# Kernel optimization log

Hardware: AMD Instinct MI355X
Metric: run time of the kernel (lower is better)

Reference implementation:

```python
import jax, jax.numpy as jnp
import numpy as np

LATENT = 256
HEADS = 4
DIM_HEAD = 256            # dim_head = latent_channels
INNER = HEADS * DIM_HEAD  # 1024
ROT_DIM = DIM_HEAD // 2   # rotary dim per coordinate (relative_emb_dim=2)
MIN_FREQ = 1.0 / 64.0     # 1/res
ROT_SCALE = 16.0          # CrossFormer scale
FF_SCALE = 0.5            # Gaussian Fourier feature scale
PI = 3.141592653589793
OUT_CH = 3


def _gelu(x):
    return jax.nn.gelu(x, approximate=False)  # torch nn.GELU default (erf)


def _rot_freqs(coords, dim):
    # coords: [b, n] -> freqs [b, n, dim]
    inv_freq = 1.0 / (10000.0 ** (jnp.arange(0, dim, 2, dtype=jnp.float32) / dim))
    t = coords * (ROT_SCALE / MIN_FREQ)
    f = t[..., None] * inv_freq               # [b, n, dim//2]
    return jnp.concatenate([f, f], axis=-1)    # [b, n, dim]


def _rotate_half(x):
    x1, x2 = jnp.split(x, 2, axis=-1)
    return jnp.concatenate([-x2, x1], axis=-1)


def _apply_rot(t, freqs):
    return t * jnp.cos(freqs) + _rotate_half(t) * jnp.sin(freqs)


def _apply_2d_rot(t, fx, fy):
    d = t.shape[-1]
    tx, ty = t[..., : d // 2], t[..., d // 2 :]
    return jnp.concatenate([_apply_rot(tx, fx), _apply_rot(ty, fy)], axis=-1)


def _inst_norm(t, eps=1e-5):
    # galerkin normalization: non-affine norm over head dim (InstanceNorm1d, affine=False)
    mu = jnp.mean(t, axis=-1, keepdims=True)
    var = jnp.var(t, axis=-1, keepdims=True)
    return (t - mu) * jax.lax.rsqrt(var + eps)


def setup_inputs() -> dict:
    key = jax.random.key(0)
    ks = jax.random.split(key, 20)
    b, nq, nc = 8, 4096, 4096
    s = 0.02
    return {
        "z": jax.random.normal(ks[0], (b, nc, LATENT), jnp.float32),
        "query_pos": jax.random.uniform(ks[1], (b, nq, 2), jnp.float32),
        "context_pos": jax.random.uniform(ks[2], (b, nc, 2), jnp.float32),
        # GaussianFourierFeatureTransform buffer B: [2, mapping_size=latent/2]
        "B_ff": jax.random.normal(ks[3], (2, LATENT // 2), jnp.float32) * FF_SCALE,
        # coordinate_projection linears (bias=False)
        "Wc1": jax.random.normal(ks[4], (LATENT, LATENT), jnp.float32) * s,
        "Wc2": jax.random.normal(ks[5], (LATENT, LATENT), jnp.float32) * s,
        # cross attention projections
        "Wq": jax.random.normal(ks[6], (LATENT, INNER), jnp.float32) * s,
        "Wkv": jax.random.normal(ks[7], (LATENT, 2 * INNER), jnp.float32) * s,
        "Wo": jax.random.normal(ks[8], (INNER, LATENT), jnp.float32) * s,
        "bo": jnp.zeros((LATENT,), jnp.float32),
        # feed-forward (mlp_dim = latent)
        "Wf1": jax.random.normal(ks[9], (LATENT, LATENT), jnp.float32) * s,
        "bf1": jnp.zeros((LATENT,), jnp.float32),
        "Wf2": jax.random.normal(ks[10], (LATENT, LATENT), jnp.float32) * s,
        "bf2": jnp.zeros((LATENT,), jnp.float32),
        # output head
        "Wh1": jax.random.normal(ks[11], (LATENT + 2, LATENT), jnp.float32) * s,
        "Wh2": jax.random.normal(ks[12], (LATENT, LATENT // 2), jnp.float32) * s,
        "Wh3": jax.random.normal(ks[13], (LATENT // 2, OUT_CH), jnp.float32) * s,
        "bh3": jnp.zeros((OUT_CH,), jnp.float32),
    }


def reference(z, query_pos, context_pos, B_ff, Wc1, Wc2, Wq, Wkv, Wo, bo,
              Wf1, bf1, Wf2, bf2, Wh1, Wh2, Wh3, bh3):
    b, nq, _ = query_pos.shape
    nc = z.shape[1]
    # 1) Gaussian Fourier features + 2-layer projection
    ff = 2.0 * PI * (query_pos @ B_ff)                           # [b, nq, latent/2]
    x = jnp.concatenate([jnp.sin(ff), jnp.cos(ff)], axis=-1)      # [b, nq, latent]
    x = _gelu(x @ Wc1) @ Wc2
    # 2) galerkin cross attention with 2D rotary relative pos emb
    q = (x @ Wq).reshape(b, nq, HEADS, DIM_HEAD).transpose(0, 2, 1, 3)
    k, v = jnp.split(z @ Wkv, 2, axis=-1)
    k = k.reshape(b, nc, HEADS, DIM_HEAD).transpose(0, 2, 1, 3)
    v = v.reshape(b, nc, HEADS, DIM_HEAD).transpose(0, 2, 1, 3)
    fxq = _rot_freqs(query_pos[..., 0], ROT_DIM)[:, None]         # [b,1,nq,rot]
    fyq = _rot_freqs(query_pos[..., 1], ROT_DIM)[:, None]
    fxk = _rot_freqs(context_pos[..., 0], ROT_DIM)[:, None]
    fyk = _rot_freqs(context_pos[..., 1], ROT_DIM)[:, None]
    q = _apply_2d_rot(q, fxq, fyq)
    k = _apply_2d_rot(k, fxk, fyk)
    k = _inst_norm(k)
    v = _inst_norm(v)
    kv = jnp.einsum('bhnd,bhne->bhde', k, v)                      # [b,h,d,d]
    attn = jnp.einsum('bhmd,bhde->bhme', q, kv) * (1.0 / nc)      # [b,h,nq,d]
    attn = attn.transpose(0, 2, 1, 3).reshape(b, nq, INNER)
    x = (attn @ Wo + bo) + x                                      # residual
    x = (_gelu(x @ Wf1 + bf1) @ Wf2 + bf2) + x                    # FFN residual
    # 3) output head on [features, coords]
    h = jnp.concatenate([x, query_pos], axis=-1)
    h = _gelu(h @ Wh1)
    h = _gelu(h @ Wh2)
    return h @ Wh3 + bh3                                          # [b, nq, out_ch]
```

## Files before the change

### kernel.cpp

```cpp
#include <hip/hip_runtime.h>
#include <math.h>


typedef unsigned short u16;
typedef __attribute__((ext_vector_type(4))) float f32x4;
typedef __attribute__((ext_vector_type(8))) short s16x8;
typedef __attribute__((ext_vector_type(8))) unsigned short u16x8;
typedef __attribute__((ext_vector_type(4))) unsigned short u16x4;

#define LOG2_1E4_D64 0.20762050593046013f

__device__ __forceinline__ u16 f2b(float f){
  union { float f; unsigned u; } v; v.f = f;
  unsigned u = v.u;
  u += 0x7FFFu + ((u >> 16) & 1u);
  return (u16)(u >> 16);
}
__device__ __forceinline__ float b2f(u16 b){
  union { unsigned u; float f; } v; v.u = ((unsigned)b) << 16; return v.f;
}
__device__ __forceinline__ float gelu_f(float x){
  return 0.5f * x * (1.0f + erff(x * 0.7071067811865475f));
}

#if __has_builtin(__builtin_amdgcn_global_load_lds)
#define HAVE_GLL 1
typedef const __attribute__((address_space(1))) void* as1cv;
typedef __attribute__((address_space(3))) void* as3v;
__device__ __forceinline__ void gload16(const void* g, void* l){
  __builtin_amdgcn_global_load_lds((as1cv)g, (as3v)l, 16, 0, 0);
}
#else
#define HAVE_GLL 0
#endif


__global__ __launch_bounds__(256) void k_cast(const float* __restrict__ in, u16* __restrict__ out){
  long i = (long)blockIdx.x * 256 + threadIdx.x;
  float4 f = ((const float4*)in)[i];
  u16x4 o = { f2b(f.x), f2b(f.y), f2b(f.z), f2b(f.w) };
  ((u16x4*)out)[i] = o;
}

struct TCArgs {
  const float* W[9]; u16* Wt[9];
  int K[9]; int N[9]; int boff[10];
};
__global__ __launch_bounds__(256) void k_tcast_all(TCArgs a){
  int b = blockIdx.x;
  int w = 0;
  while (b >= a.boff[w+1]) w++;
  int idx = (b - a.boff[w]) * 256 + threadIdx.x;
  int K = a.K[w], N = a.N[w];
  int n = idx / K, k = idx - n * K;
  a.Wt[w][idx] = f2b(a.W[w][(long)k * N + n]);
}

__global__ __launch_bounds__(256) void k_fourier(const float* __restrict__ qp, const float* __restrict__ Bff, u16* __restrict__ X0){
  int tid = threadIdx.x;
  long r = (long)blockIdx.x * 2 + (tid >> 7);
  int j = tid & 127;
  float qx = qp[r*2], qy = qp[r*2+1];
  float ff = 6.283185307179586f * (qx * Bff[j] + qy * Bff[128 + j]);
  X0[r*256 + j]       = f2b(sinf(ff));
  X0[r*256 + 128 + j] = f2b(cosf(ff));
}

__global__ __launch_bounds__(256) void k_rot_q(u16* __restrict__ Q, const float* __restrict__ qp){
  int id = blockIdx.x * 256 + threadIdx.x;
  int l = id & 63;
  int h = (id >> 6) & 3;
  long r = (unsigned)id >> 8;
  float invf = exp2f(-(float)l * LOG2_1E4_D64);
  float ax = qp[r*2]   * 1024.0f * invf;
  float ay = qp[r*2+1] * 1024.0f * invf;
  float sx = sinf(ax), cx = cosf(ax), sy = sinf(ay), cy = cosf(ay);
  long base = r*1024 + (long)h*256 + l;
  float t0 = b2f(Q[base]), t1 = b2f(Q[base+64]), t2 = b2f(Q[base+128]), t3 = b2f(Q[base+192]);
  Q[base]       = f2b(t0*cx - t1*sx);
  Q[base + 64]  = f2b(t1*cx + t0*sx);
  Q[base + 128] = f2b(t2*cy - t3*sy);
  Q[base + 192] = f2b(t3*cy + t2*sy);
}

__global__ __launch_bounds__(256) void k_kvt(const u16* __restrict__ in, const float* __restrict__ cp,
                                             u16* __restrict__ outT, int do_rot){
  __shared__ u16 sb[64*256];
  int tid  = threadIdx.x;
  int lane = tid & 63, wave = tid >> 6;
  int h = blockIdx.y;
  long n0 = (long)blockIdx.x * 64;
  int bb  = (int)(n0 >> 12);
  int nn0 = (int)(n0 & 4095);
  float invf = exp2f(-(float)lane * LOG2_1E4_D64);

  for (int rr = 0; rr < 16; rr++){
    int lrow = wave * 16 + rr;
    long n = n0 + lrow;
    long base = n * 1024 + (long)h * 256 + lane;
    float r0 = b2f(in[base]), r1 = b2f(in[base+64]), r2 = b2f(in[base+128]), r3 = b2f(in[base+192]);
    if (do_rot){
      float ax = cp[n*2]   * 1024.0f * invf;
      float ay = cp[n*2+1] * 1024.0f * invf;
      float sx = sinf(ax), cxv = cosf(ax), sy = sinf(ay), cyv = cosf(ay);
      float t0 = r0, t1 = r1, t2 = r2, t3 = r3;
      r0 = t0*cxv - t1*sx;  r1 = t1*cxv + t0*sx;
      r2 = t2*cyv - t3*sy;  r3 = t3*cyv + t2*sy;
    }
    float s1 = r0+r1+r2+r3;
    float s2 = r0*r0+r1*r1+r2*r2+r3*r3;
#pragma unroll
    for (int m = 1; m < 64; m <<= 1){ s1 += __shfl_xor(s1, m, 64); s2 += __shfl_xor(s2, m, 64); }
    float mu  = s1 * 0.00390625f;
    float var = s2 * 0.00390625f - mu*mu;
    float inv = 1.0f / sqrtf(var + 1e-5f);
    int sw = (lrow >> 2) << 1;
    sb[lrow*256 + ((lane      ) ^ sw)] = f2b((r0-mu)*inv);
    sb[lrow*256 + ((lane + 64 ) ^ sw)] = f2b((r1-mu)*inv);
    sb[lrow*256 + ((lane + 128) ^ sw)] = f2b((r2-mu)*inv);
    sb[lrow*256 + ((lane + 192) ^ sw)] = f2b((r3-mu)*inv);
  }
  __syncthreads();
  long matbase = ((long)(bb*4 + h) * 256) * 4096 + nn0;
  int n4 = (lane & 15) * 4;
  int sw = (lane & 15) << 1;
#pragma unroll
  for (int rnd = 0; rnd < 16; rnd++){
    int d = rnd*16 + wave*4 + (lane >> 4);
    u16x4 vv;
#pragma unroll
    for (int j = 0; j < 4; j++) vv[j] = sb[(n4+j)*256 + (d ^ sw)];
    *(u16x4*)(outT + matbase + (long)d*4096 + n4) = vv;
  }
}

__global__ __launch_bounds__(256) void k_red(const float* __restrict__ p, u16* __restrict__ out, long stride){
  long i = (long)blockIdx.x * 256 + threadIdx.x;
  f32x4 s = ((const f32x4*)p)[i];
  s += ((const f32x4*)(p + stride))[i];
  s += ((const f32x4*)(p + 2*stride))[i];
  s += ((const f32x4*)(p + 3*stride))[i];
  u16x4 o = { f2b(s[0]), f2b(s[1]), f2b(s[2]), f2b(s[3]) };
  ((u16x4*)out)[i] = o;
}

__global__ __launch_bounds__(256) void k_final(const u16* __restrict__ H2, const float* __restrict__ Wh3,
                                               const float* __restrict__ bh3, float* __restrict__ out){
  long r = (long)blockIdx.x * 256 + threadIdx.x;
  float a0 = bh3[0], a1 = bh3[1], a2 = bh3[2];
  const u16x8* hrow = (const u16x8*)(H2 + r*128);
#pragma unroll
  for (int c8 = 0; c8 < 16; c8++){
    u16x8 hv = hrow[c8];
#pragma unroll
    for (int e = 0; e < 8; e++){
      float f = b2f(hv[e]);
      int k = c8*8 + e;
      a0 += f * Wh3[k*3];
      a1 += f * Wh3[k*3+1];
      a2 += f * Wh3[k*3+2];
    }
  }
  out[r*3] = a0; out[r*3+1] = a1; out[r*3+2] = a2;
}


enum { EP_B = 0, EP_GELU = 1, EP_BIAS_GELU = 2, EP_BIAS_RESB = 3, EP_SCALE = 4,
       EP_T = 5, EP_QP_GELU = 6, EP_TF32 = 7 };

struct GArgs {
  const u16* A; const u16* B;
  u16* Cb; float* Cf;
  const float* bias; const u16* res; const float* qp; const float* wtail;
  float scale;
  int M, N, K, lda, ldb, ldc, NLO;
  long sAh, sAl, sBh, sBl, sCh, sCl;
};

template<int EP>
__global__ __launch_bounds__(256, 2)
void gemm_k(GArgs g){
  int z = blockIdx.z;
  int zh = z / g.NLO, zl = z - zh * g.NLO;
  const u16* A = g.A + (long)zh * g.sAh + (long)zl * g.sAl;
  const u16* B = g.B + (long)zh * g.sBh + (long)zl * g.sBl;
  long coff = (long)zh * g.sCh + (long)zl * g.sCl;

  __shared__ u16 As[128*32];
  __shared__ u16 Bs[128*32];

  int tid  = threadIdx.x;
  int lane = tid & 63;
  int wave = tid >> 6;
  int wm = (wave & 1) << 6;
  int wn = (wave >> 1) << 6;
  long m0 = (long)blockIdx.x * 128;
  long n0 = (long)blockIdx.y * 128;

  int r15 = lane & 15;
  int cc  = lane >> 4;

#if HAVE_GLL
  int rA0 = (wave*2 + 0) * 16;
  int rA1 = (wave*2 + 1) * 16;
  int srow = lane >> 2;
  int scol = (lane & 3) * 8;
  u16* lA0 = &As[rA0*32];
  u16* lA1 = &As[rA1*32];
  u16* lB0 = &Bs[rA0*32];
  u16* lB1 = &Bs[rA1*32];
  const u16* gA0 = A + (m0 + rA0 + srow) * g.lda + scol;
  const u16* gA1 = A + (m0 + rA1 + srow) * g.lda + scol;
  const u16* gB0 = B + (n0 + rA0 + srow) * g.ldb + scol;
  const u16* gB1 = B + (n0 + rA1 + srow) * g.ldb + scol;
#else
  int sm  = tid >> 2;
  int sc  = tid & 3;
  int so0 = sm * 32 + sc * 8;
  int so1 = (sm + 64) * 32 + sc * 8;
  const u16* pA0 = A + (m0 + sm ) * g.lda + sc * 8;
  const u16* pA1 = A + (m0 + sm + 64) * g.lda + sc * 8;
  const u16* pB0 = B + (n0 + sm ) * g.ldb + sc * 8;
  const u16* pB1 = B + (n0 + sm + 64) * g.ldb + sc * 8;
#endif

  f32x4 acc[4][4];
#pragma unroll
  for (int i = 0; i < 4; i++)
#pragma unroll
    for (int j = 0; j < 4; j++)
      acc[i][j] = f32x4{0.f, 0.f, 0.f, 0.f};

  for (int k0 = 0; k0 < g.K; k0 += 32){
#if HAVE_GLL
    __syncthreads();
    gload16(gA0 + k0, lA0);
    gload16(gA1 + k0, lA1);
    gload16(gB0 + k0, lB0);
    gload16(gB1 + k0, lB1);
    __syncthreads();
#else
    u16x8 va0 = *(const u16x8*)(pA0 + k0);
    u16x8 va1 = *(const u16x8*)(pA1 + k0);
    u16x8 vb0 = *(const u16x8*)(pB0 + k0);
    u16x8 vb1 = *(const u16x8*)(pB1 + k0);
    __syncthreads();
    *(u16x8*)&As[so0] = va0;
    *(u16x8*)&As[so1] = va1;
    *(u16x8*)&Bs[so0] = vb0;
    *(u16x8*)&Bs[so1] = vb1;
    __syncthreads();
#endif
    s16x8 af[4], bf[4];
#pragma unroll
    for (int i = 0; i < 4; i++) af[i] = *(const s16x8*)&As[(wm + i*16 + r15)*32 + cc*8];
#pragma unroll
    for (int i = 0; i < 4; i++) bf[i] = *(const s16x8*)&Bs[(wn + i*16 + r15)*32 + cc*8];
#pragma unroll
    for (int i = 0; i < 4; i++)
#pragma unroll
      for (int j = 0; j < 4; j++)
        acc[i][j] = __builtin_amdgcn_mfma_f32_16x16x32_bf16(af[i], bf[j], acc[i][j], 0, 0, 0);
  }

  int colb = (int)n0 + wn + r15;
  int rowb = (int)m0 + wm + cc * 4;
#pragma unroll
  for (int i = 0; i < 4; i++){
#pragma unroll
    for (int j = 0; j < 4; j++){
      int col = colb + j*16;
#pragma unroll
      for (int r = 0; r < 4; r++){
        int row = rowb + i*16 + r;
        float v = acc[i][j][r];
        if constexpr (EP == EP_B){
          g.Cb[coff + (long)row * g.ldc + col] = f2b(v);
        } else if constexpr (EP == EP_GELU){
          g.Cb[coff + (long)row * g.ldc + col] = f2b(gelu_f(v));
        } else if constexpr (EP == EP_BIAS_GELU){
          v = gelu_f(v + g.bias[col]);
          g.Cb[coff + (long)row * g.ldc + col] = f2b(v);
        } else if constexpr (EP == EP_BIAS_RESB){
          v += g.bias[col] + b2f(g.res[(long)row * g.ldc + col]);
          g.Cb[coff + (long)row * g.ldc + col] = f2b(v);
        } else if constexpr (EP == EP_SCALE){
          g.Cb[coff + (long)row * g.ldc + col] = f2b(v * g.scale);
        } else if constexpr (EP == EP_T){
          g.Cb[coff + (long)col * g.ldc + row] = f2b(v);
        } else if constexpr (EP == EP_TF32){
          g.Cf[coff + (long)col * g.ldc + row] = v;
        } else {
          v += g.qp[(long)row*2] * g.wtail[col] + g.qp[(long)row*2+1] * g.wtail[256+col];
          g.Cb[coff + (long)row * g.ldc + col] = f2b(gelu_f(v));
        }
      }
    }
  }
}


extern "C" void kernel_launch(void* const* d_in, const int* in_sizes, int n_in,
                              void* d_out, int out_size, void* d_ws, size_t ws_size,
                              hipStream_t stream){
  const float* z   = (const float*)d_in[0];
  const float* qp  = (const float*)d_in[1];
  const float* cp  = (const float*)d_in[2];
  const float* Bff = (const float*)d_in[3];
  const float* Wc1 = (const float*)d_in[4];
  const float* Wc2 = (const float*)d_in[5];
  const float* Wq  = (const float*)d_in[6];
  const float* Wkv = (const float*)d_in[7];
  const float* Wo  = (const float*)d_in[8];
  const float* bo  = (const float*)d_in[9];
  const float* Wf1 = (const float*)d_in[10];
  const float* bf1 = (const float*)d_in[11];
  const float* Wf2 = (const float*)d_in[12];
  const float* bf2 = (const float*)d_in[13];
  const float* Wh1 = (const float*)d_in[14];
  const float* Wh2 = (const float*)d_in[15];
  const float* Wh3 = (const float*)d_in[16];
  const float* bh3 = (const float*)d_in[17];
  float* out = (float*)d_out;
  (void)in_sizes; (void)n_in; (void)out_size;

  size_t mb = ws_size >> 20;
  int C;
  if      (mb >= 264) C = 1;
  else if (mb >= 168) C = 2;
  else if (mb >= 120) C = 4;
  else                C = 8;
  const int NB = 8 / C;
  const long R = (long)NB * 4096;

  char* ws = (char*)d_ws;
  const size_t MB = 1024*1024;
  u16* WqT  = (u16*)(ws + 0);
  u16* WkvT = (u16*)(ws + 512*1024);
  u16* WoT  = (u16*)(ws + 1536*1024);
  u16* Wc1T = (u16*)(ws + 2048*1024);
  u16* Wc2T = (u16*)(ws + (2048+128)*1024);
  u16* Wf1T = (u16*)(ws + (2048+256)*1024);
  u16* Wf2T = (u16*)(ws + (2048+384)*1024);
  u16* Wh1T = (u16*)(ws + (2048+512)*1024);
  u16* Wh2T = (u16*)(ws + (2048+640)*1024);
  u16* R1 = (u16*)(ws + 4*MB);
  u16* R2 = (u16*)(ws + 20*MB);
  u16* R3 = (u16*)(ws + 36*MB);
  u16* R4 = (u16*)(ws + 52*MB);
  u16* kvT = (u16*)(ws + 68*MB);
  u16* BIG1 = (u16*)(ws + 72*MB);
  u16* BIG2 = (u16*)((char*)BIG1 + (size_t)NB*8*MB);
  u16* BIG3 = (u16*)((char*)BIG2 + (size_t)NB*8*MB);

  u16* X0b = R1; u16* X2b = R1;
  u16* Tb  = R2; u16* H1b = R2;
  u16* Xb  = R3;
  u16* Zb  = R4; u16* H2b = R4;

  auto G = [&](int ep, const u16* A, const u16* B, u16* Cb, float* Cf,
               const float* bias, const u16* res, const float* qq, const float* wtail,
               float scale, int M, int N, int K, int lda, int ldb, int ldc,
               int nz, int NLO, long sAh, long sAl, long sBh, long sBl, long sCh, long sCl){
    GArgs g;
    g.A=A; g.B=B; g.Cb=Cb; g.Cf=Cf; g.bias=bias; g.res=res; g.qp=qq; g.wtail=wtail;
    g.scale=scale; g.M=M; g.N=N; g.K=K; g.lda=lda; g.ldb=ldb; g.ldc=ldc; g.NLO=NLO;
    g.sAh=sAh; g.sAl=sAl; g.sBh=sBh; g.sBl=sBl; g.sCh=sCh; g.sCl=sCl;
    dim3 gr(M/128, N/128, nz); dim3 bl(256);
    switch(ep){
      case EP_B:          gemm_k<EP_B><<<gr,bl,0,stream>>>(g); break;
      case EP_GELU:       gemm_k<EP_GELU><<<gr,bl,0,stream>>>(g); break;
      case EP_BIAS_GELU:  gemm_k<EP_BIAS_GELU><<<gr,bl,0,stream>>>(g); break;
      case EP_BIAS_RESB:  gemm_k<EP_BIAS_RESB><<<gr,bl,0,stream>>>(g); break;
      case EP_SCALE:      gemm_k<EP_SCALE><<<gr,bl,0,stream>>>(g); break;
      case EP_T:          gemm_k<EP_T><<<gr,bl,0,stream>>>(g); break;
      case EP_QP_GELU:    gemm_k<EP_QP_GELU><<<gr,bl,0,stream>>>(g); break;
      case EP_TF32:       gemm_k<EP_TF32><<<gr,bl,0,stream>>>(g); break;
    }
  };

  k_cast<<<dim3(8192), dim3(256), 0, stream>>>(z, Zb);
  {
    TCArgs a;
    const float* Ws[9] = { Wq, Wkv, Wo, Wc1, Wc2, Wf1, Wf2, Wh1, Wh2 };
    u16* Wts[9] = { WqT, WkvT, WoT, Wc1T, Wc2T, Wf1T, Wf2T, Wh1T, Wh2T };
    int Ks[9] = { 256, 256, 1024, 256, 256, 256, 256, 256, 256 };
    int Ns[9] = { 1024, 2048, 256, 256, 256, 256, 256, 256, 128 };
    int off = 0;
    for (int i = 0; i < 9; i++){
      a.W[i] = Ws[i]; a.Wt[i] = Wts[i]; a.K[i] = Ks[i]; a.N[i] = Ns[i];
      a.boff[i] = off; off += Ks[i]*Ns[i]/256;
    }
    a.boff[9] = off;
    k_tcast_all<<<dim3(off), dim3(256), 0, stream>>>(a);
  }

  k_fourier<<<dim3(16384), dim3(256), 0, stream>>>(qp, Bff, X0b);
  G(EP_GELU, X0b, Wc1T, Tb, 0, 0,0,0,0, 1.f, 32768,256,256, 256,256,256, 1,1, 0,0,0,0,0,0);
  G(EP_B,    Tb,  Wc2T, Xb, 0, 0,0,0,0, 1.f, 32768,256,256, 256,256,256, 1,1, 0,0,0,0,0,0);

  for (int c = 0; c < C; c++){
    long row0 = (long)c * R;
    const u16* Zc = Zb + row0 * 256;
    G(EP_B, Zc, WkvT, BIG1, 0, 0,0,0,0, 1.f, (int)R,1024,256, 256,256,1024, 1,1, 0,0,0,0,0,0);
    k_kvt<<<dim3((int)(R/64), 4), dim3(256), 0, stream>>>(BIG1, cp + row0*2, BIG2, 1);
    G(EP_B, Zc, WkvT + 1024*256, BIG1, 0, 0,0,0,0, 1.f, (int)R,1024,256, 256,256,1024, 1,1, 0,0,0,0,0,0);
    k_kvt<<<dim3((int)(R/64), 4), dim3(256), 0, stream>>>(BIG1, cp + row0*2, BIG3, 0);
    G(EP_TF32, BIG2, BIG3, 0, (float*)BIG1, 0,0,0,0, 1.f,
      256,256,1024, 4096,4096,256, 4*NB*4, NB*4,
      1024,1048576, 1024,1048576, (long)NB*4*65536,65536);
    k_red<<<dim3(NB*256), dim3(256), 0, stream>>>((float*)BIG1, kvT + (long)c*NB*4*65536, (long)NB*4*65536);
    G(EP_B, Xb + row0*256, WqT, BIG1, 0, 0,0,0,0, 1.f, (int)R,1024,256, 256,256,1024, 1,1, 0,0,0,0,0,0);
    k_rot_q<<<dim3((int)R), dim3(256), 0, stream>>>(BIG1, qp + row0*2);
    G(EP_SCALE, BIG1, kvT + (long)c*NB*4*65536, BIG2, 0, 0,0,0,0, 1.0f/4096.0f,
      4096,256,256, 1024,256,1024, NB*4,4, 4194304,256, 262144,65536, 4194304,256);
    G(EP_BIAS_RESB, BIG2, WoT, X2b + row0*256, 0, bo, Xb + row0*256, 0,0, 1.f,
      (int)R,256,1024, 1024,1024,256, 1,1, 0,0,0,0,0,0);
  }

  G(EP_BIAS_GELU, X2b, Wf1T, Tb, 0, bf1, 0,0,0, 1.f, 32768,256,256, 256,256,256, 1,1, 0,0,0,0,0,0);
  G(EP_BIAS_RESB, Tb, Wf2T, Xb, 0, bf2, X2b, 0,0, 1.f, 32768,256,256, 256,256,256, 1,1, 0,0,0,0,0,0);
  G(EP_QP_GELU, Xb, Wh1T, H1b, 0, 0,0, qp, Wh1 + 65536, 1.f, 32768,256,256, 256,256,256, 1,1, 0,0,0,0,0,0);
  G(EP_GELU, H1b, Wh2T, H2b, 0, 0,0,0,0, 1.f, 32768,128,256, 256,256,128, 1,1, 0,0,0,0,0,0);
  k_final<<<dim3(128), dim3(256), 0, stream>>>(H2b, Wh3, bh3, out);
}
```

Measured before the change: 648.2 us.

## Fuse K/V/Q projections with rotary, instance norm and transpose epilogues

Adds a gemm_fuse kernel that computes a full 256-wide head tile per block, so the rotary embedding and the per-row instance norm can be applied in registers. For K and V it writes the transposed layout directly, and for Q it writes the rotated result. This removes the separate k_kvt and k_rot_q passes and their intermediate global round trips. The kv GEMM now uses a non-transposed fp32 epilogue with its operand order swapped. The trade-offs are larger shared memory and register use per block, which may lower occupancy, and the switch to fast __sinf/__cosf on large angles, which may cost accuracy.

```diff
diff --git a/kernel.cpp b/kernel.cpp
--- a/kernel.cpp
+++ b/kernel.cpp
@@ -66,74 +66,6 @@
   X0[r*256 + 128 + j] = f2b(cosf(ff));
 }
 
-__global__ __launch_bounds__(256) void k_rot_q(u16* __restrict__ Q, const float* __restrict__ qp){
-  int id = blockIdx.x * 256 + threadIdx.x;
-  int l = id & 63;
-  int h = (id >> 6) & 3;
-  long r = (unsigned)id >> 8;
-  float invf = exp2f(-(float)l * LOG2_1E4_D64);
-  float ax = qp[r*2]   * 1024.0f * invf;
-  float ay = qp[r*2+1] * 1024.0f * invf;
-  float sx = sinf(ax), cx = cosf(ax), sy = sinf(ay), cy = cosf(ay);
-  long base = r*1024 + (long)h*256 + l;
-  float t0 = b2f(Q[base]), t1 = b2f(Q[base+64]), t2 = b2f(Q[base+128]), t3 = b2f(Q[base+192]);
-  Q[base]       = f2b(t0*cx - t1*sx);
-  Q[base + 64]  = f2b(t1*cx + t0*sx);
-  Q[base + 128] = f2b(t2*cy - t3*sy);
-  Q[base + 192] = f2b(t3*cy + t2*sy);
-}
-
-__global__ __launch_bounds__(256) void k_kvt(const u16* __restrict__ in, const float* __restrict__ cp,
-                                             u16* __restrict__ outT, int do_rot){
-  __shared__ u16 sb[64*256];
-  int tid  = threadIdx.x;
-  int lane = tid & 63, wave = tid >> 6;
-  int h = blockIdx.y;
-  long n0 = (long)blockIdx.x * 64;
-  int bb  = (int)(n0 >> 12);
-  int nn0 = (int)(n0 & 4095);
-  float invf = exp2f(-(float)lane * LOG2_1E4_D64);
-
-  for (int rr = 0; rr < 16; rr++){
-    int lrow = wave * 16 + rr;
-    long n = n0 + lrow;
-    long base = n * 1024 + (long)h * 256 + lane;
-    float r0 = b2f(in[base]), r1 = b2f(in[base+64]), r2 = b2f(in[base+128]), r3 = b2f(in[base+192]);
-    if (do_rot){
-      float ax = cp[n*2]   * 1024.0f * invf;
-      float ay = cp[n*2+1] * 1024.0f * invf;
-      float sx = sinf(ax), cxv = cosf(ax), sy = sinf(ay), cyv = cosf(ay);
-      float t0 = r0, t1 = r1, t2 = r2, t3 = r3;
-      r0 = t0*cxv - t1*sx;  r1 = t1*cxv + t0*sx;
-      r2 = t2*cyv - t3*sy;  r3 = t3*cyv + t2*sy;
-    }
-    float s1 = r0+r1+r2+r3;
-    float s2 = r0*r0+r1*r1+r2*r2+r3*r3;
-#pragma unroll
-    for (int m = 1; m < 64; m <<= 1){ s1 += __shfl_xor(s1, m, 64); s2 += __shfl_xor(s2, m, 64); }
-    float mu  = s1 * 0.00390625f;
-    float var = s2 * 0.00390625f - mu*mu;
-    float inv = 1.0f / sqrtf(var + 1e-5f);
-    int sw = (lrow >> 2) << 1;
-    sb[lrow*256 + ((lane      ) ^ sw)] = f2b((r0-mu)*inv);
-    sb[lrow*256 + ((lane + 64 ) ^ sw)] = f2b((r1-mu)*inv);
-    sb[lrow*256 + ((lane + 128) ^ sw)] = f2b((r2-mu)*inv);
-    sb[lrow*256 + ((lane + 192) ^ sw)] = f2b((r3-mu)*inv);
-  }
-  __syncthreads();
-  long matbase = ((long)(bb*4 + h) * 256) * 4096 + nn0;
-  int n4 = (lane & 15) * 4;
-  int sw = (lane & 15) << 1;
-#pragma unroll
-  for (int rnd = 0; rnd < 16; rnd++){
-    int d = rnd*16 + wave*4 + (lane >> 4);
-    u16x4 vv;
-#pragma unroll
-    for (int j = 0; j < 4; j++) vv[j] = sb[(n4+j)*256 + (d ^ sw)];
-    *(u16x4*)(outT + matbase + (long)d*4096 + n4) = vv;
-  }
-}
-
 __global__ __launch_bounds__(256) void k_red(const float* __restrict__ p, u16* __restrict__ out, long stride){
   long i = (long)blockIdx.x * 256 + threadIdx.x;
   f32x4 s = ((const f32x4*)p)[i];
@@ -165,8 +97,208 @@
 }
 
 
+template<int MODE>
+__global__ __launch_bounds__(256, 2)
+void gemm_fuse(const u16* __restrict__ A, const u16* __restrict__ Bw,
+               u16* __restrict__ out, const float* __restrict__ pos){
+  __shared__ u16 As[128*32];
+  __shared__ u16 Bs[256*32];
+
+  int tid  = threadIdx.x;
+  int lane = tid & 63;
+  int wave = tid >> 6;
+  int wm = (wave & 1) << 6;
+  int wn = (wave >> 1) << 7;
+  int whalf = wave >> 1;
+  int h = blockIdx.y;
+  long m0 = (long)blockIdx.x * 128;
+
+  int r15 = lane & 15;
+  int cc  = lane >> 4;
+  const u16* Bh = Bw + (long)h * 65536;
+
+#if HAVE_GLL
+  int srow = lane >> 2;
+  int scol = (lane & 3) * 8;
+  u16* lA[2]; const u16* gA[2];
+#pragma unroll
+  for (int t = 0; t < 2; t++){
+    int rb = (wave*2 + t) * 16;
+    lA[t] = &As[rb*32];
+    gA[t] = A + (m0 + rb + srow) * 256 + scol;
+  }
+  u16* lB[4]; const u16* gB[4];
+#pragma unroll
+  for (int t = 0; t < 4; t++){
+    int rb = (wave*4 + t) * 16;
+    lB[t] = &Bs[rb*32];
+    gB[t] = Bh + (rb + srow) * 256 + scol;
+  }
+#else
+  int sm  = tid >> 2;
+  int sc  = tid & 3;
+#endif
+
+  f32x4 acc[4][8];
+#pragma unroll
+  for (int i = 0; i < 4; i++)
+#pragma unroll
+    for (int j = 0; j < 8; j++)
+      acc[i][j] = f32x4{0.f, 0.f, 0.f, 0.f};
+
+  for (int k0 = 0; k0 < 256; k0 += 32){
+#if HAVE_GLL
+    __syncthreads();
+#pragma unroll
+    for (int t = 0; t < 2; t++) gload16(gA[t] + k0, lA[t]);
+#pragma unroll
+    for (int t = 0; t < 4; t++) gload16(gB[t] + k0, lB[t]);
+    __syncthreads();
+#else
+    u16x8 va = *(const u16x8*)(A + (m0 + sm)*256 + sc*8 + k0);
+    u16x8 vb0 = *(const u16x8*)(Bh + (sm      )*256 + sc*8 + k0);
+    u16x8 vb1 = *(const u16x8*)(Bh + (sm + 64 )*256 + sc*8 + k0);
+    u16x8 vb2 = *(const u16x8*)(Bh + (sm + 128)*256 + sc*8 + k0);
+    u16x8 vb3 = *(const u16x8*)(Bh + (sm + 192)*256 + sc*8 + k0);
+    u16x8 va1 = *(const u16x8*)(A + (m0 + sm + 64)*256 + sc*8 + k0);
+    __syncthreads();
+    *(u16x8*)&As[sm*32 + sc*8] = va;
+    *(u16x8*)&As[(sm+64)*32 + sc*8] = va1;
+    *(u16x8*)&Bs[sm*32 + sc*8] = vb0;
+    *(u16x8*)&Bs[(sm+64)*32 + sc*8] = vb1;
+    *(u16x8*)&Bs[(sm+128)*32 + sc*8] = vb2;
+    *(u16x8*)&Bs[(sm+192)*32 + sc*8] = vb3;
+    __syncthreads();
+#endif
+    s16x8 af[4], bf[8];
+#pragma unroll
+    for (int i = 0; i < 4; i++) af[i] = *(const s16x8*)&As[(wm + i*16 + r15)*32 + cc*8];
+#pragma unroll
+    for (int j = 0; j < 8; j++) bf[j] = *(const s16x8*)&Bs[(wn + j*16 + r15)*32 + cc*8];
+#pragma unroll
+    for (int i = 0; i < 4; i++)
+#pragma unroll
+      for (int j = 0; j < 8; j++)
+        acc[i][j] = __builtin_amdgcn_mfma_f32_16x16x32_bf16(af[i], bf[j], acc[i][j], 0, 0, 0);
+  }
+
+  if constexpr (MODE != 1){
+    float invf4[4];
+#pragma unroll
+    for (int jl = 0; jl < 4; jl++)
+      invf4[jl] = 1024.0f * exp2f(-(float)(jl*16 + r15) * LOG2_1E4_D64);
+#pragma unroll
+    for (int i = 0; i < 4; i++){
+#pragma unroll
+      for (int r = 0; r < 4; r++){
+        long n = m0 + wm + i*16 + cc*4 + r;
+        float p = pos[n*2 + whalf];
+#pragma unroll
+        for (int jl = 0; jl < 4; jl++){
+          float a = p * invf4[jl];
+          float s = __sinf(a), c = __cosf(a);
+          float t0 = acc[i][jl][r], t1 = acc[i][jl+4][r];
+          acc[i][jl][r]   = t0*c - t1*s;
+          acc[i][jl+4][r] = t1*c + t0*s;
+        }
+      }
+    }
+  }
+
+  if constexpr (MODE == 2){
+#pragma unroll
+    for (int i = 0; i < 4; i++)
+#pragma unroll
+      for (int j = 0; j < 8; j++)
+#pragma unroll
+        for (int r = 0; r < 4; r++){
+          long row = m0 + wm + i*16 + cc*4 + r;
+          int col = h*256 + wn + j*16 + r15;
+          out[row*1024 + col] = f2b(acc[i][j][r]);
+        }
+  } else {
+    __shared__ float PS1[2][128];
+    __shared__ float PS2[2][128];
+    __shared__ u16 TB[64*256];
+
+    float s1a[4][4], s2a[4][4];
+#pragma unroll
+    for (int i = 0; i < 4; i++){
+#pragma unroll
+      for (int r = 0; r < 4; r++){
+        float s1 = 0.f, s2 = 0.f;
+#pragma unroll
+        for (int j = 0; j < 8; j++){
+          float v = acc[i][j][r];
+          s1 += v; s2 += v*v;
+        }
+#pragma unroll
+        for (int m = 1; m < 16; m <<= 1){
+          s1 += __shfl_xor(s1, m, 64);
+          s2 += __shfl_xor(s2, m, 64);
+        }
+        s1a[i][r] = s1; s2a[i][r] = s2;
+        int rowid = (wave&1)*64 + i*16 + cc*4 + r;
+        if (r15 == 0){ PS1[whalf][rowid] = s1; PS2[whalf][rowid] = s2; }
+      }
+    }
+    __syncthreads();
+#pragma unroll
+    for (int i = 0; i < 4; i++){
+#pragma unroll
+      for (int r = 0; r < 4; r++){
+        int rowid = (wave&1)*64 + i*16 + cc*4 + r;
+        float s1 = PS1[0][rowid] + PS1[1][rowid];
+        float s2 = PS2[0][rowid] + PS2[1][rowid];
+        float mu  = s1 * 0.00390625f;
+        float var = s2 * 0.00390625f - mu*mu;
+        float inv = 1.0f / sqrtf(var + 1e-5f);
+#pragma unroll
+        for (int j = 0; j < 8; j++)
+          acc[i][j] = f32x4{ (acc[i][j][0+0]-0.f), acc[i][j][1], acc[i][j][2], acc[i][j][3] },
+          acc[i][j][r] = (acc[i][j][r] - mu) * inv;
+      }
+    }
+    __syncthreads();
+
+    int bb  = (int)(m0 >> 12);
+    int nn0 = (int)(m0 & 4095);
+    long matbase = ((long)(bb*4 + h) * 256) * 4096;
+#pragma unroll
+    for (int p = 0; p < 2; p++){
+      if ((wave & 1) == p){
+#pragma unroll
+        for (int i = 0; i < 4; i++)
+#pragma unroll
+          for (int j = 0; j < 8; j++)
+#pragma unroll
+            for (int r = 0; r < 4; r++){
+              int nl = i*16 + cc*4 + r;
+              int d  = wn + j*16 + r15;
+              TB[nl*256 + (d ^ ((nl>>2)<<1))] = f2b(acc[i][j][r]);
+            }
+      }
+      __syncthreads();
+      {
+        int n4 = (lane & 15) * 4;
+        int sw = (lane & 15) << 1;
+#pragma unroll
+        for (int rnd = 0; rnd < 16; rnd++){
+          int d = rnd*16 + wave*4 + (lane >> 4);
+          u16x4 vv;
+#pragma unroll
+          for (int jj = 0; jj < 4; jj++) vv[jj] = TB[(n4+jj)*256 + (d ^ sw)];
+          *(u16x4*)(out + matbase + (long)d*4096 + nn0 + p*64 + n4) = vv;
+        }
+      }
+      __syncthreads();
+    }
+  }
+}
+
+
 enum { EP_B = 0, EP_GELU = 1, EP_BIAS_GELU = 2, EP_BIAS_RESB = 3, EP_SCALE = 4,
-       EP_T = 5, EP_QP_GELU = 6, EP_TF32 = 7 };
+       EP_QP_GELU = 5, EP_F32 = 6 };
 
 struct GArgs {
   const u16* A; const u16* B;
@@ -286,10 +418,8 @@
           g.Cb[coff + (long)row * g.ldc + col] = f2b(v);
         } else if constexpr (EP == EP_SCALE){
           g.Cb[coff + (long)row * g.ldc + col] = f2b(v * g.scale);
-        } else if constexpr (EP == EP_T){
-          g.Cb[coff + (long)col * g.ldc + row] = f2b(v);
-        } else if constexpr (EP == EP_TF32){
-          g.Cf[coff + (long)col * g.ldc + row] = v;
+        } else if constexpr (EP == EP_F32){
+          g.Cf[coff + (long)row * g.ldc + col] = v;
         } else {
           v += g.qp[(long)row*2] * g.wtail[col] + g.qp[(long)row*2+1] * g.wtail[256+col];
           g.Cb[coff + (long)row * g.ldc + col] = f2b(gelu_f(v));
@@ -373,9 +503,8 @@
       case EP_BIAS_GELU:  gemm_k<EP_BIAS_GELU><<<gr,bl,0,stream>>>(g); break;
       case EP_BIAS_RESB:  gemm_k<EP_BIAS_RESB><<<gr,bl,0,stream>>>(g); break;
       case EP_SCALE:      gemm_k<EP_SCALE><<<gr,bl,0,stream>>>(g); break;
-      case EP_T:          gemm_k<EP_T><<<gr,bl,0,stream>>>(g); break;
       case EP_QP_GELU:    gemm_k<EP_QP_GELU><<<gr,bl,0,stream>>>(g); break;
-      case EP_TF32:       gemm_k<EP_TF32><<<gr,bl,0,stream>>>(g); break;
+      case EP_F32:        gemm_k<EP_F32><<<gr,bl,0,stream>>>(g); break;
     }
   };
 
@@ -402,16 +531,13 @@
   for (int c = 0; c < C; c++){
     long row0 = (long)c * R;
     const u16* Zc = Zb + row0 * 256;
-    G(EP_B, Zc, WkvT, BIG1, 0, 0,0,0,0, 1.f, (int)R,1024,256, 256,256,1024, 1,1, 0,0,0,0,0,0);
-    k_kvt<<<dim3((int)(R/64), 4), dim3(256), 0, stream>>>(BIG1, cp + row0*2, BIG2, 1);
-    G(EP_B, Zc, WkvT + 1024*256, BIG1, 0, 0,0,0,0, 1.f, (int)R,1024,256, 256,256,1024, 1,1, 0,0,0,0,0,0);
-    k_kvt<<<dim3((int)(R/64), 4), dim3(256), 0, stream>>>(BIG1, cp + row0*2, BIG3, 0);
-    G(EP_TF32, BIG2, BIG3, 0, (float*)BIG1, 0,0,0,0, 1.f,
+    gemm_fuse<0><<<dim3((int)(R/128), 4), dim3(256), 0, stream>>>(Zc, WkvT, BIG2, cp + row0*2);
+    gemm_fuse<1><<<dim3((int)(R/128), 4), dim3(256), 0, stream>>>(Zc, WkvT + 1024*256, BIG3, cp + row0*2);
+    G(EP_F32, BIG3, BIG2, 0, (float*)BIG1, 0,0,0,0, 1.f,
       256,256,1024, 4096,4096,256, 4*NB*4, NB*4,
       1024,1048576, 1024,1048576, (long)NB*4*65536,65536);
     k_red<<<dim3(NB*256), dim3(256), 0, stream>>>((float*)BIG1, kvT + (long)c*NB*4*65536, (long)NB*4*65536);
-    G(EP_B, Xb + row0*256, WqT, BIG1, 0, 0,0,0,0, 1.f, (int)R,1024,256, 256,256,1024, 1,1, 0,0,0,0,0,0);
-    k_rot_q<<<dim3((int)R), dim3(256), 0, stream>>>(BIG1, qp + row0*2);
+    gemm_fuse<2><<<dim3((int)(R/128), 4), dim3(256), 0, stream>>>(Xb + row0*256, WqT, BIG1, qp + row0*2);
     G(EP_SCALE, BIG1, kvT + (long)c*NB*4*65536, BIG2, 0, 0,0,0,0, 1.0f/4096.0f,
       4096,256,256, 1024,256,1024, NB*4,4, 4194304,256, 262144,65536, 4194304,256);
     G(EP_BIAS_RESB, BIG2, WoT, X2b + row0*256, 0, bo, Xb + row0*256, 0,0, 1.f,
```

Result: faster. 603.1 us (-7.0%).
